# Kernel tuning notes

Measured on AMD Instinct MI355X. Metric: run time of the kernel, lower is better.

The kernel has to match this reference:

```python
import jax, jax.numpy as jnp
import numpy as np

N_NODES = 50000
N_EDGES = 1_600_000
IN_DIM = 128
HID = 64


def gcn_conv(x, src, dst, w, W, b, n):
    # PyG GCNConv(normalize=True, add_self_loops=True):
    # add self loops with weight 1, sym-normalize, x@W (no bias in lin), scatter-add, +bias
    loop = jnp.arange(n)
    s = jnp.concatenate([src, loop])
    d = jnp.concatenate([dst, loop])
    ww = jnp.concatenate([w, jnp.ones((n,), w.dtype)])
    deg = jax.ops.segment_sum(ww, d, num_segments=n)                 # [n]
    dis = jnp.where(deg > 0, jax.lax.rsqrt(deg), 0.0)                # deg^{-1/2}, inf->0
    norm = dis[s] * ww * dis[d]                                      # [E+n]
    h = x @ W                                                        # [n, out]
    msg = h[s] * norm[:, None]                                       # gather + scale
    out = jax.ops.segment_sum(msg, d, num_segments=n)                # scatter-add at dst
    return out + b


def setup_inputs() -> dict:
    key = jax.random.key(0)
    ks = jax.random.split(key, 9)
    X = jax.random.normal(ks[0], (N_NODES, IN_DIM), dtype=jnp.float32)
    edge_index = jax.random.randint(ks[1], (2, N_EDGES), 0, N_NODES, dtype=jnp.int64)
    edge_weight = jax.random.uniform(ks[2], (N_EDGES,), dtype=jnp.float32)
    s1 = 1.0 / np.sqrt(IN_DIM)
    s2 = 1.0 / np.sqrt(HID)
    W1 = jax.random.uniform(ks[3], (IN_DIM, HID), jnp.float32, -s1, s1)
    b1 = jax.random.uniform(ks[4], (HID,), jnp.float32, -s1, s1)
    W2 = jax.random.uniform(ks[5], (HID, HID), jnp.float32, -s2, s2)
    b2 = jax.random.uniform(ks[6], (HID,), jnp.float32, -s2, s2)
    Wl = jax.random.uniform(ks[7], (HID, 1), jnp.float32, -s2, s2)
    bl = jax.random.uniform(ks[8], (1,), jnp.float32, -s2, s2)
    return {"X": X, "edge_index": edge_index, "edge_weight": edge_weight,
            "W1": W1, "b1": b1, "W2": W2, "b2": b2, "Wl": Wl, "bl": bl}


def reference(X, edge_index, edge_weight, W1, b1, W2, b2, Wl, bl):
    n = X.shape[0]
    src, dst = edge_index[0], edge_index[1]
    h = jax.nn.relu(gcn_conv(X, src, dst, edge_weight, W1, b1, n))
    # F.dropout(p=0.2) is identity in eval mode
    h = jax.nn.relu(gcn_conv(h, src, dst, edge_weight, W2, b2, n))
    return jax.nn.sigmoid(h @ Wl + bl).squeeze(1)   # [n]
```

## Files before the change

### kernel.cpp

```cpp
#include <hip/hip_runtime.h>

typedef float f32x2 __attribute__((ext_vector_type(2)));

#define A2B 512
#define A2T 512
#define STG 3200

__device__ __forceinline__ long ld_idx(const void* idx, long pos, int is64) {
  return is64 ? (long)((const long long*)idx)[pos]
              : (long)((const int*)idx)[pos];
}

__device__ __forceinline__ int detect_is64(const void* idx) {
  const unsigned long long* p = (const unsigned long long*)idx;
  unsigned long long v = p[threadIdx.x & 63];
  return (__ballot((v >> 32) != 0ull) == 0ull) ? 1 : 0;
}

__device__ __forceinline__ uint4 pack16_fp8(const float* acc) {
  uint4 o;
  unsigned v;
  v = 0;
  v = __builtin_amdgcn_cvt_pk_fp8_f32(acc[0],  acc[1],  v, false);
  v = __builtin_amdgcn_cvt_pk_fp8_f32(acc[2],  acc[3],  v, true);
  o.x = v; v = 0;
  v = __builtin_amdgcn_cvt_pk_fp8_f32(acc[4],  acc[5],  v, false);
  v = __builtin_amdgcn_cvt_pk_fp8_f32(acc[6],  acc[7],  v, true);
  o.y = v; v = 0;
  v = __builtin_amdgcn_cvt_pk_fp8_f32(acc[8],  acc[9],  v, false);
  v = __builtin_amdgcn_cvt_pk_fp8_f32(acc[10], acc[11], v, true);
  o.z = v; v = 0;
  v = __builtin_amdgcn_cvt_pk_fp8_f32(acc[12], acc[13], v, false);
  v = __builtin_amdgcn_cvt_pk_fp8_f32(acc[14], acc[15], v, true);
  o.w = v;
  return o;
}

__global__ __launch_bounds__(256) void k_front(const void* __restrict__ idx,
                                               unsigned* __restrict__ histT,
                                               long E, int chunk, unsigned M,
                                               const float* __restrict__ X,
                                               const float* __restrict__ W1,
                                               unsigned char* __restrict__ h, int n) {
  __shared__ float smem[2048];
  const int t = threadIdx.x;
  if (blockIdx.x < A2B) {
    unsigned* cnt = (unsigned*)smem;
    const int b = blockIdx.x;
    const int is64 = detect_is64(idx);
    cnt[t] = 0;
    __syncthreads();
    const long e0 = (long)b * chunk;
    long e1 = e0 + chunk; if (e1 > E) e1 = E;
    for (long e = e0 + t; e < e1; e += 256) {
      unsigned d = (unsigned)ld_idx(idx, E + e, is64);
      atomicAdd(&cnt[__umulhi(d, M)], 1u);
    }
    __syncthreads();
    histT[(size_t)t * A2B + b] = cnt[t];
    return;
  }
  float* Ws = smem;
  for (int i = t; i < 2048; i += 256)
    ((float4*)Ws)[i] = ((const float4*)W1)[i];
  __syncthreads();
  int gid = (blockIdx.x - A2B) * 256 + t;
  int node = gid >> 2;
  int fg = (gid & 3) * 16;
  if (node >= n) return;
  const float4* xr4 = (const float4*)(X + (size_t)node * 128);
  float acc[16];
#pragma unroll
  for (int f = 0; f < 16; ++f) acc[f] = 0.0f;
  for (int k4 = 0; k4 < 32; ++k4) {
    float4 x = xr4[k4];
#pragma unroll
    for (int kk = 0; kk < 4; ++kk) {
      float xv = (kk == 0) ? x.x : (kk == 1) ? x.y : (kk == 2) ? x.z : x.w;
      const float4* wrow = (const float4*)(Ws + (k4 * 4 + kk) * 64 + fg);
#pragma unroll
      for (int f4 = 0; f4 < 4; ++f4) {
        float4 w = wrow[f4];
        acc[f4 * 4 + 0] = fmaf(xv, w.x, acc[f4 * 4 + 0]);
        acc[f4 * 4 + 1] = fmaf(xv, w.y, acc[f4 * 4 + 1]);
        acc[f4 * 4 + 2] = fmaf(xv, w.z, acc[f4 * 4 + 2]);
        acc[f4 * 4 + 3] = fmaf(xv, w.w, acc[f4 * 4 + 3]);
      }
    }
  }
  *(uint4*)(h + (size_t)node * 64 + fg) = pack16_fp8(acc);
}

__global__ __launch_bounds__(256) void k_colscan(const unsigned* __restrict__ histT,
                                                 unsigned* __restrict__ baseT,
                                                 unsigned* __restrict__ colsum) {
  __shared__ unsigned sh[256];
  const int k = blockIdx.x, t = threadIdx.x;
  const uint2 v = ((const uint2*)(histT + (size_t)k * A2B))[t];
  unsigned s = v.x + v.y;
  sh[t] = s;
  __syncthreads();
  for (int off = 1; off < 256; off <<= 1) {
    unsigned u = (t >= off) ? sh[t - off] : 0;
    __syncthreads();
    sh[t] += u;
    __syncthreads();
  }
  unsigned excl = sh[t] - s;
  uint2 o; o.x = excl; o.y = excl + v.x;
  ((uint2*)(baseT + (size_t)k * A2B))[t] = o;
  if (t == 255) colsum[k] = sh[255];
}

__global__ __launch_bounds__(A2T) void k_bucket(const void* __restrict__ idx,
                                                const float* __restrict__ w,
                                                const unsigned* __restrict__ baseT,
                                                const unsigned* __restrict__ colsum,
                                                uint2* __restrict__ recs,
                                                long E, int chunk, unsigned M) {
  __shared__ uint2 stage[STG];
  __shared__ unsigned cnt[256], lofs[256], lbase[256], bcol[256], scanb[256];
  const int b = blockIdx.x, t = threadIdx.x;
  const long e0 = (long)b * chunk;
  long e1 = e0 + chunk; if (e1 > E) e1 = E;
  const int m = (int)(e1 - e0);
  const int is64 = detect_is64(idx);
  if (t < 256) scanb[t] = colsum[t];
  __syncthreads();
  for (int off = 1; off < 256; off <<= 1) {
    unsigned u = 0;
    if (t < 256 && t >= off) u = scanb[t - off];
    __syncthreads();
    if (t < 256) scanb[t] += u;
    __syncthreads();
  }
  if (t < 256) {
    bcol[t] = (scanb[t] - colsum[t]) + baseT[(size_t)t * A2B + b];
    cnt[t] = 0;
  }
  __syncthreads();
  unsigned short dc[8]; unsigned char kc[8];
  int nk = 0;
  for (long e = e0 + t; e < e1; e += A2T, ++nk) {
    unsigned d = (unsigned)ld_idx(idx, E + e, is64);
    unsigned kb = __umulhi(d, M);
    dc[nk] = (unsigned short)d; kc[nk] = (unsigned char)kb;
    atomicAdd(&cnt[kb], 1u);
  }
  __syncthreads();
  if (t < 256) scanb[t] = cnt[t];
  __syncthreads();
  for (int off = 1; off < 256; off <<= 1) {
    unsigned u = 0;
    if (t < 256 && t >= off) u = scanb[t - off];
    __syncthreads();
    if (t < 256) scanb[t] += u;
    __syncthreads();
  }
  if (t < 256) { unsigned ex = scanb[t] - cnt[t]; lbase[t] = ex; lofs[t] = ex; }
  __syncthreads();
  nk = 0;
  for (long e = e0 + t; e < e1; e += A2T, ++nk) {
    unsigned s = (unsigned)ld_idx(idx, e, is64);
    float wv = w[e];
    unsigned kb = kc[nk];
    unsigned pos = atomicAdd(&lofs[kb], 1u);
    stage[pos] = make_uint2(s | ((unsigned)dc[nk] << 16), __float_as_uint(wv));
  }
  __syncthreads();
  for (int i = t; i < m; i += A2T) {
    uint2 r = stage[i];
    unsigned kb = __umulhi(r.x >> 16, M);
    recs[bcol[kb] + (unsigned)i - lbase[kb]] = r;
  }
}

__global__ __launch_bounds__(1024) void k_build(const uint2* __restrict__ recs,
                                                const unsigned* __restrict__ colsum,
                                                int* __restrict__ rowptr,
                                                float* __restrict__ dis,
                                                float2* __restrict__ edges,
                                                int n, int dwidth, long E) {
  __shared__ float wsum[256];
  __shared__ unsigned cnt[256], lofs[256], scanb[256];
  __shared__ int shr0, shr1;
  const int k = blockIdx.x, t = threadIdx.x;
  const int d0 = k * dwidth;
  if (t < 256) scanb[t] = colsum[t];
  __syncthreads();
  for (int off = 1; off < 256; off <<= 1) {
    unsigned u = 0;
    if (t < 256 && t >= off) u = scanb[t - off];
    __syncthreads();
    if (t < 256) scanb[t] += u;
    __syncthreads();
  }
  if (t == k) { shr1 = (int)scanb[t]; shr0 = (int)(scanb[t] - colsum[t]); }
  if (t < 256) { wsum[t] = 0.0f; cnt[t] = 0; }
  __syncthreads();
  const int r0 = shr0, r1 = shr1;
  const int m = r1 - r0;
  for (int i = t; i < m; i += 1024) {
    uint2 r = recs[r0 + i];
    int dl = (int)(r.x >> 16) - d0;
    atomicAdd(&cnt[dl], 1u);
    atomicAdd(&wsum[dl], __uint_as_float(r.y));
  }
  __syncthreads();
  if (t < 256) scanb[t] = cnt[t];
  __syncthreads();
  for (int off = 1; off < 256; off <<= 1) {
    unsigned u = 0;
    if (t < 256 && t >= off) u = scanb[t - off];
    __syncthreads();
    if (t < 256) scanb[t] += u;
    __syncthreads();
  }
  if (t < 256) {
    unsigned ex = scanb[t] - cnt[t];
    lofs[t] = (unsigned)r0 + ex;
    int d = d0 + t;
    if (t < dwidth && d < n) {
      rowptr[d] = r0 + (int)ex;
      dis[d] = rsqrtf(1.0f + wsum[t]);
    }
  }
  if (k == gridDim.x - 1 && t == 0) rowptr[n] = (int)E;
  __syncthreads();
  for (int i = t; i < m; i += 1024) {
    uint2 r = recs[r0 + i];
    unsigned pos = atomicAdd(&lofs[(int)(r.x >> 16) - d0], 1u);
    edges[pos] = make_float2(__uint_as_float(r.x & 0xffffu), __uint_as_float(r.y));
  }
}

__device__ __forceinline__ void gather_acc(const unsigned char* __restrict__ h,
                                           const float* __restrict__ dis,
                                           const float2* __restrict__ edges,
                                           int beg, int end, float s0,
                                           int half, int l32, int fl, int eg,
                                           float* acc) {
  f32x2 a0 = {0.0f, 0.0f}, a1 = {0.0f, 0.0f}, a2 = {0.0f, 0.0f}, a3 = {0.0f, 0.0f};
  for (int base = beg; base < end; base += 32) {
    int m = end - base; if (m > 32) m = 32;
    float2 pk = (l32 < m) ? edges[base + l32] : make_float2(__int_as_float(0), 0.0f);
    float nrm = dis[__float_as_int(pk.x)] * pk.y * s0;
    int   sj[8];
    float nj[8];
#pragma unroll
    for (int s = 0; s < 8; ++s) {
      int j = half * 32 + s * 4 + eg;
      sj[s] = __float_as_int(__shfl(pk.x, j));
      nj[s] = __shfl(nrm, j);
    }
    uint2 hv[8];
#pragma unroll
    for (int s = 0; s < 8; ++s)
      hv[s] = *(const uint2*)(h + (size_t)sj[s] * 64 + fl * 8);
#pragma unroll
    for (int s = 0; s < 8; ++s) {
      f32x2 nj2 = {nj[s], nj[s]};
      a0 += __builtin_amdgcn_cvt_pk_f32_fp8(hv[s].x, false) * nj2;
      a1 += __builtin_amdgcn_cvt_pk_f32_fp8(hv[s].x, true)  * nj2;
      a2 += __builtin_amdgcn_cvt_pk_f32_fp8(hv[s].y, false) * nj2;
      a3 += __builtin_amdgcn_cvt_pk_f32_fp8(hv[s].y, true)  * nj2;
    }
  }
  acc[0] = a0[0]; acc[1] = a0[1]; acc[2] = a1[0]; acc[3] = a1[1];
  acc[4] = a2[0]; acc[5] = a2[1]; acc[6] = a3[0]; acc[7] = a3[1];
#pragma unroll
  for (int off = 8; off < 32; off <<= 1)
#pragma unroll
    for (int i = 0; i < 8; ++i) acc[i] += __shfl_xor(acc[i], off);
}

__device__ __forceinline__ void add_bias_self(const unsigned char* __restrict__ h,
                                              const float* __restrict__ b,
                                              int node, int fl, float s0, float* acc) {
  uint2 hv = *(const uint2*)(h + (size_t)node * 64 + fl * 8);
  f32x2 q0 = __builtin_amdgcn_cvt_pk_f32_fp8(hv.x, false);
  f32x2 q1 = __builtin_amdgcn_cvt_pk_f32_fp8(hv.x, true);
  f32x2 q2 = __builtin_amdgcn_cvt_pk_f32_fp8(hv.y, false);
  f32x2 q3 = __builtin_amdgcn_cvt_pk_f32_fp8(hv.y, true);
  float hs[8] = {q0[0], q0[1], q1[0], q1[1], q2[0], q2[1], q3[0], q3[1]};
  float4 bv0 = *(const float4*)(b + fl * 8);
  float4 bv1 = *(const float4*)(b + fl * 8 + 4);
  float bb[8] = {bv0.x, bv0.y, bv0.z, bv0.w, bv1.x, bv1.y, bv1.z, bv1.w};
  float s2 = s0 * s0;
#pragma unroll
  for (int i = 0; i < 8; ++i) acc[i] += bb[i] + hs[i] * s2;
}

__global__ __launch_bounds__(256) void k_gather_mid(const unsigned char* __restrict__ h,
                                                    const float* __restrict__ dis,
                                                    const float2* __restrict__ edges,
                                                    const int* __restrict__ rowptr,
                                                    const float* __restrict__ b1,
                                                    const float* __restrict__ W2,
                                                    unsigned char* __restrict__ h2, int n) {
  __shared__ float W2s[64 * 64];
  __shared__ float xs[8 * 64];
  const int t = threadIdx.x;
  for (int i = t; i < 1024; i += 256)
    ((float4*)W2s)[i] = ((const float4*)W2)[i];
  int lane = t & 63;
  int half = lane >> 5;
  int l32 = lane & 31;
  int fl = lane & 7;
  int eg = (lane >> 3) & 3;
  int nl = t >> 5;
  int node = blockIdx.x * 8 + nl;
  int beg = 0, end = 0; float s0 = 0.0f;
  if (node < n) { beg = rowptr[node]; end = rowptr[node + 1]; s0 = dis[node]; }
  float acc[8];
  gather_acc(h, dis, edges, beg, end, s0, half, l32, fl, eg, acc);
  if (node < n) {
    add_bias_self(h, b1, node, fl, s0, acc);
    if (eg == 0) {
#pragma unroll
      for (int i = 0; i < 8; ++i) xs[nl * 64 + fl * 8 + i] = fmaxf(acc[i], 0.0f);
    }
  }
  __syncthreads();
  int tl = l32;
  int node2 = blockIdx.x * 8 + (t >> 5);
  if (node2 >= n) return;
  const float* xrow = xs + (t >> 5) * 64;
  int f = tl * 2;
  float a0 = 0.0f, a1 = 0.0f;
#pragma unroll 8
  for (int k = 0; k < 64; ++k) {
    float xk = xrow[k];
    f32x2 wv = *(const f32x2*)(W2s + k * 64 + f);
    a0 = fmaf(xk, wv[0], a0);
    a1 = fmaf(xk, wv[1], a1);
  }
  unsigned v = __builtin_amdgcn_cvt_pk_fp8_f32(a0, a1, 0u, false);
  *(unsigned short*)(h2 + (size_t)node2 * 64 + f) = (unsigned short)v;
}

__global__ __launch_bounds__(256) void k_gather_fin(const unsigned char* __restrict__ h,
                                                    const float* __restrict__ dis,
                                                    const float2* __restrict__ edges,
                                                    const int* __restrict__ rowptr,
                                                    const float* __restrict__ b2,
                                                    const float* __restrict__ Wl,
                                                    const float* __restrict__ bl,
                                                    float* __restrict__ out, int n) {
  int lane = threadIdx.x & 63;
  int half = lane >> 5;
  int l32 = lane & 31;
  int fl = lane & 7;
  int eg = (lane >> 3) & 3;
  int node = blockIdx.x * 8 + (int)(threadIdx.x >> 5);
  if (node >= n) return;
  int beg = rowptr[node], end = rowptr[node + 1];
  float s0 = dis[node];
  float acc[8];
  gather_acc(h, dis, edges, beg, end, s0, half, l32, fl, eg, acc);
  add_bias_self(h, b2, node, fl, s0, acc);
  float4 wl0 = *(const float4*)(Wl + fl * 8);
  float4 wl1 = *(const float4*)(Wl + fl * 8 + 4);
  float wl[8] = {wl0.x, wl0.y, wl0.z, wl0.w, wl1.x, wl1.y, wl1.z, wl1.w};
  float v = 0.0f;
#pragma unroll
  for (int i = 0; i < 8; ++i) v += fmaxf(acc[i], 0.0f) * wl[i];
#pragma unroll
  for (int off = 1; off < 8; off <<= 1) v += __shfl_xor(v, off);
  if (l32 == 0) out[node] = 1.0f / (1.0f + expf(-(v + bl[0])));
}

extern "C" void kernel_launch(void* const* d_in, const int* in_sizes, int n_in,
                              void* d_out, int out_size, void* d_ws, size_t ws_size,
                              hipStream_t stream) {
  const float* X  = (const float*)d_in[0];
  const void*  EI = d_in[1];
  const float* EW = (const float*)d_in[2];
  const float* W1 = (const float*)d_in[3];
  const float* b1 = (const float*)d_in[4];
  const float* W2 = (const float*)d_in[5];
  const float* b2 = (const float*)d_in[6];
  const float* Wl = (const float*)d_in[7];
  const float* bl = (const float*)d_in[8];
  float* out = (float*)d_out;

  const int  n = in_sizes[0] / 128;
  const long E = (long)in_sizes[1] / 2;

  const int chunk  = (int)((E + A2B - 1) / A2B);
  const int dwidth = (n + 255) / 256;
  const unsigned M = (unsigned)((0x100000000ULL + (unsigned)dwidth - 1) / (unsigned)dwidth);

  auto align = [](size_t x) { return (x + 255) & ~(size_t)255; };
  char* ws = (char*)d_ws;
  size_t off = 0;
  float*         dis    = (float*)(ws + off);         off += align((size_t)n * 4);
  int*           rowptr = (int*)(ws + off);           off += align((size_t)(n + 1) * 4);
  unsigned*      colsum = (unsigned*)(ws + off);      off += align(256 * 4);
  unsigned*      histT  = (unsigned*)(ws + off);      off += align((size_t)A2B * 256 * 4);
  unsigned*      baseT  = (unsigned*)(ws + off);      off += align((size_t)A2B * 256 * 4);
  uint2*         recs   = (uint2*)(ws + off);         off += align((size_t)E * 8);
  float2*        edges  = (float2*)(ws + off);        off += align((size_t)E * 8);
  unsigned char* A      = (unsigned char*)(ws + off); off += align((size_t)n * 64);
  unsigned char* A2     = (unsigned char*)(ws + off); off += align((size_t)n * 64);

  const int nbW = (n + 7) / 8;
  const int nbG = (n * 4 + 255) / 256;

  k_front<<<A2B + nbG, dim3(256), 0, stream>>>(EI, histT, E, chunk, M, X, W1, A, n);
  k_colscan<<<256, 256, 0, stream>>>(histT, baseT, colsum);
  k_bucket<<<A2B, A2T, 0, stream>>>(EI, EW, baseT, colsum, recs, E, chunk, M);
  k_build<<<256, 1024, 0, stream>>>(recs, colsum, rowptr, dis, edges, n, dwidth, E);

  k_gather_mid<<<nbW, dim3(256), 0, stream>>>(A, dis, edges, rowptr, b1, W2, A2, n);
  k_gather_fin<<<nbW, dim3(256), 0, stream>>>(A2, dis, edges, rowptr, b2, Wl, bl, out, n);
}
```

Before: 210.3 us.

## Prenormalize edge weights by source degree and drop shuffles in gather

Adds a k_norm pass that multiplies each CSR edge weight by dis[src] once, so the two gather kernels no longer look up dis per edge. Within a node, edges are read directly per lane (clamped index plus a mask) instead of being loaded once and broadcast with shuffles. The destination scale s0 is applied after accumulation. This costs an extra launch plus a read and write of the 1.6M-edge array, and each edge record is now loaded by several lanes.

```diff
diff --git a/kernel.cpp b/kernel.cpp
--- a/kernel.cpp
+++ b/kernel.cpp
@@ -234,32 +234,38 @@
   }
 }
 
+__global__ __launch_bounds__(256) void k_norm(float2* __restrict__ edges,
+                                              const float* __restrict__ dis, long E) {
+  long i0 = (long)blockIdx.x * 256 + threadIdx.x;
+  long stride = (long)gridDim.x * 256;
+  for (long i = i0; i < E; i += stride) {
+    float2 r = edges[i];
+    r.y *= dis[__float_as_int(r.x)];
+    edges[i] = r;
+  }
+}
+
 __device__ __forceinline__ void gather_acc(const unsigned char* __restrict__ h,
-                                           const float* __restrict__ dis,
                                            const float2* __restrict__ edges,
-                                           int beg, int end, float s0,
-                                           int half, int l32, int fl, int eg,
+                                           int beg, int end, int eg, int fl,
                                            float* acc) {
   f32x2 a0 = {0.0f, 0.0f}, a1 = {0.0f, 0.0f}, a2 = {0.0f, 0.0f}, a3 = {0.0f, 0.0f};
+  const unsigned char* hf = h + fl * 8;
   for (int base = beg; base < end; base += 32) {
-    int m = end - base; if (m > 32) m = 32;
-    float2 pk = (l32 < m) ? edges[base + l32] : make_float2(__int_as_float(0), 0.0f);
-    float nrm = dis[__float_as_int(pk.x)] * pk.y * s0;
-    int   sj[8];
-    float nj[8];
+    float2 rv[8];
 #pragma unroll
     for (int s = 0; s < 8; ++s) {
-      int j = half * 32 + s * 4 + eg;
-      sj[s] = __float_as_int(__shfl(pk.x, j));
-      nj[s] = __shfl(nrm, j);
+      int idx = base + s * 4 + eg;
+      rv[s] = edges[min(idx, end - 1)];
     }
     uint2 hv[8];
 #pragma unroll
     for (int s = 0; s < 8; ++s)
-      hv[s] = *(const uint2*)(h + (size_t)sj[s] * 64 + fl * 8);
+      hv[s] = *(const uint2*)(hf + (size_t)__float_as_int(rv[s].x) * 64);
 #pragma unroll
     for (int s = 0; s < 8; ++s) {
-      f32x2 nj2 = {nj[s], nj[s]};
+      float w = (base + s * 4 + eg < end) ? rv[s].y : 0.0f;
+      f32x2 nj2 = {w, w};
       a0 += __builtin_amdgcn_cvt_pk_f32_fp8(hv[s].x, false) * nj2;
       a1 += __builtin_amdgcn_cvt_pk_f32_fp8(hv[s].x, true)  * nj2;
       a2 += __builtin_amdgcn_cvt_pk_f32_fp8(hv[s].y, false) * nj2;
@@ -304,7 +310,6 @@
   for (int i = t; i < 1024; i += 256)
     ((float4*)W2s)[i] = ((const float4*)W2)[i];
   int lane = t & 63;
-  int half = lane >> 5;
   int l32 = lane & 31;
   int fl = lane & 7;
   int eg = (lane >> 3) & 3;
@@ -313,8 +318,10 @@
   int beg = 0, end = 0; float s0 = 0.0f;
   if (node < n) { beg = rowptr[node]; end = rowptr[node + 1]; s0 = dis[node]; }
   float acc[8];
-  gather_acc(h, dis, edges, beg, end, s0, half, l32, fl, eg, acc);
+  gather_acc(h, edges, beg, end, eg, fl, acc);
   if (node < n) {
+#pragma unroll
+    for (int i = 0; i < 8; ++i) acc[i] *= s0;
     add_bias_self(h, b1, node, fl, s0, acc);
     if (eg == 0) {
 #pragma unroll
@@ -348,7 +355,6 @@
                                                     const float* __restrict__ bl,
                                                     float* __restrict__ out, int n) {
   int lane = threadIdx.x & 63;
-  int half = lane >> 5;
   int l32 = lane & 31;
   int fl = lane & 7;
   int eg = (lane >> 3) & 3;
@@ -357,7 +363,9 @@
   int beg = rowptr[node], end = rowptr[node + 1];
   float s0 = dis[node];
   float acc[8];
-  gather_acc(h, dis, edges, beg, end, s0, half, l32, fl, eg, acc);
+  gather_acc(h, edges, beg, end, eg, fl, acc);
+#pragma unroll
+  for (int i = 0; i < 8; ++i) acc[i] *= s0;
   add_bias_self(h, b2, node, fl, s0, acc);
   float4 wl0 = *(const float4*)(Wl + fl * 8);
   float4 wl1 = *(const float4*)(Wl + fl * 8 + 4);
@@ -406,11 +414,13 @@
 
   const int nbW = (n + 7) / 8;
   const int nbG = (n * 4 + 255) / 256;
+  const int nbN = 2048;
 
   k_front<<<A2B + nbG, dim3(256), 0, stream>>>(EI, histT, E, chunk, M, X, W1, A, n);
   k_colscan<<<256, 256, 0, stream>>>(histT, baseT, colsum);
   k_bucket<<<A2B, A2T, 0, stream>>>(EI, EW, baseT, colsum, recs, E, chunk, M);
   k_build<<<256, 1024, 0, stream>>>(recs, colsum, rowptr, dis, edges, n, dwidth, E);
+  k_norm<<<nbN, dim3(256), 0, stream>>>(edges, dis, E);
 
   k_gather_mid<<<nbW, dim3(256), 0, stream>>>(A, dis, edges, rowptr, b1, W2, A2, n);
   k_gather_fin<<<nbW, dim3(256), 0, stream>>>(A2, dis, edges, rowptr, b2, Wl, bl, out, n);
```

New measurement: 218.7 us. +4.0%, slower.
